# Kernel tuning notes

Hardware: AMD Instinct MI355X
Metric: run time of the kernel (lower is better)

Reference implementation:

```python
import jax, jax.numpy as jnp
import numpy as np

RADIUS = 5
KERNEL_SIZE = 2 * RADIUS - 1  # 9
PAD = KERNEL_SIZE // 2        # 4
H, W = 2048, 2048


def make_distance_kernel():
    center = RADIUS - 1
    y, x = jnp.meshgrid(jnp.arange(KERNEL_SIZE), jnp.arange(KERNEL_SIZE), indexing='ij')
    d = jnp.sqrt((x - center).astype(jnp.float32) ** 2 + (y - center).astype(jnp.float32) ** 2)
    return d.at[center, center].set(0.0)


def setup_inputs() -> dict:
    key = jax.random.key(0)
    target = (jax.random.uniform(key, (5, H, W)) < 0.15).astype(jnp.float32)
    distance_kernel = make_distance_kernel()
    return {"target": target, "distance_kernel": distance_kernel}


def _contour_weights(target, kernel):
    combined = (target.sum(axis=0) > 0).astype(jnp.float32)          # [H, W]
    padded = jnp.pad(combined, PAD, mode='edge')                      # replicate pad
    min_d = jnp.full_like(combined, jnp.inf)
    inf = jnp.float32(jnp.inf)
    for i in range(KERNEL_SIZE):
        for j in range(KERNEL_SIZE):
            if i == PAD and j == PAD:
                continue
            shifted = padded[i:i + H, j:j + W]
            diff = (shifted != combined).astype(jnp.float32)
            dist = jnp.where(diff > 0, kernel[i, j] / (diff + 1e-10), inf)
            min_d = jnp.minimum(min_d, dist)
    return jnp.where(min_d < inf, 1.0 / (min_d + 1e-10), 0.0)


def reference(target, distance_kernel):
    feature_weight = target.sum(axis=0)                               # [H, W]
    contour = _contour_weights(target, distance_kernel)
    weights = (feature_weight + contour) ** 2
    weights = (weights - weights.min()) / (weights.max() - weights.min() + 1e-10)
    return weights * (target.sum(axis=0) > 0).astype(jnp.float32)
```

## Files before the change

### kernel.cpp

```cpp
#include <hip/hip_runtime.h>
#include <stdint.h>

#define HH 2048
#define WW 2048
#define NPIX (HH*WW)
#define MROW (WW/32)
#define TSX 64
#define TSY 32
#define NBLK ((WW/TSX)*(HH/TSY))

__global__ __launch_bounds__(256) void fw_kernel(
    const float* __restrict__ target, uint8_t* __restrict__ fw,
    uint32_t* __restrict__ mask)
{
    __shared__ uint8_t nib[256];
    const int t = threadIdx.x;
    const int i = blockIdx.x * 256 + t;
    const float4* t4 = (const float4*)target;
    float4 a = t4[i];
    float4 b = t4[(NPIX/4) + i];
    float4 c = t4[2*(NPIX/4) + i];
    float4 d = t4[3*(NPIX/4) + i];
    float4 e = t4[4*(NPIX/4) + i];
    uchar4 o;
    o.x = (unsigned char)(a.x + b.x + c.x + d.x + e.x);
    o.y = (unsigned char)(a.y + b.y + c.y + d.y + e.y);
    o.z = (unsigned char)(a.z + b.z + c.z + d.z + e.z);
    o.w = (unsigned char)(a.w + b.w + c.w + d.w + e.w);
    ((uchar4*)fw)[i] = o;
    nib[t] = (uint8_t)((o.x ? 1u : 0u) | (o.y ? 2u : 0u) | (o.z ? 4u : 0u) | (o.w ? 8u : 0u));
    __syncthreads();
    if (t < 32) {
        const uint8_t* p = nib + t * 8;
        uint32_t w = 0;
        #pragma unroll
        for (int k = 0; k < 8; ++k) w |= (uint32_t)p[k] << (4 * k);
        mask[blockIdx.x * 32 + t] = w;
    }
}

__global__ __launch_bounds__(256) void contour_kernel(
    const uint8_t* __restrict__ fw, const uint32_t* __restrict__ mask,
    const float* __restrict__ dk,
    uint8_t* __restrict__ wcode, float* __restrict__ pmin, float* __restrict__ pmax)
{
    __shared__ uint32_t maskw[TSY + 8][4];
    __shared__ uint8_t  lutm2[512];
    __shared__ float    inv_ext[101];
    __shared__ float    redmn[4], redmx[4];

    const int t   = threadIdx.x;
    const int gx0 = blockIdx.x * TSX;
    const int gy0 = blockIdx.y * TSY;

    if (t < 101) inv_ext[t] = 0.0f;
    for (int idx = t; idx < 512; idx += 256) {
        uint32_t rev = __builtin_bitreverse32((uint32_t)idx) >> 23;
        uint32_t g = ((((uint32_t)idx | rev) >> 4) & 0x1Fu) | 0x100u;
        uint32_t mk = (uint32_t)__builtin_ctz(g);
        lutm2[idx] = (uint8_t)(mk * mk);
    }
    const int w0 = gx0 >> 5;
    if (t < (TSY + 8) * 4) {
        int hr = t >> 2, wc = t & 3;
        int gy = gy0 - 4 + hr; gy = min(max(gy, 0), HH - 1);
        const uint32_t* rowp = mask + gy * MROW;
        int wi = w0 - 1 + wc;
        uint32_t v;
        if (wi < 0)            v = (rowp[0] & 1u) ? 0xFFFFFFFFu : 0u;
        else if (wi > MROW-1)  v = (rowp[MROW-1] >> 31) ? 0xFFFFFFFFu : 0u;
        else                   v = rowp[wi];
        maskw[hr][wc] = v;
    }
    __syncthreads();
    if (t < 81) {
        int iy = t / 9, jx = t - (t / 9) * 9;
        int dy = iy - 4, dx = jx - 4;
        int d2 = dy * dy + dx * dx;
        if (d2 != 0)
            inv_ext[d2] = 1.0f / (dk[t] / (1.0f + 1e-10f) + 1e-10f);
    }
    __syncthreads();

    const int rl  = t >> 3;
    const int xg  = t & 7;
    const int gy  = gy0 + rl;
    const int gxb = gx0 + xg * 8;

    uint32_t fwlo = *(const uint32_t*)(fw + gy * WW + gxb);
    uint32_t fwhi = *(const uint32_t*)(fw + gy * WW + gxb + 4);

    const int pos  = xg * 8 + 28;
    const int wsel = pos >> 5;
    const uint32_t sh = (uint32_t)(pos & 31);
    uint32_t wrow[9];
    #pragma unroll
    for (int k = 0; k < 9; ++k) {
        uint64_t v = (((uint64_t)maskw[rl + k][wsel + 1]) << 32) | maskw[rl + k][wsel];
        wrow[k] = (uint32_t)(v >> sh);
    }
    uint32_t orx[4], andx[4];
    #pragma unroll
    for (int k = 1; k <= 4; ++k) {
        orx[k-1]  = wrow[4 - k] | wrow[4 + k];
        andx[k-1] = wrow[4 - k] & wrow[4 + k];
    }

    float lmn = __int_as_float(0x7F800000);
    float lmx = 0.0f;
    uint32_t outb0 = 0, outb1 = 0;

    #pragma unroll
    for (int j = 0; j < 8; ++j) {
        uint32_t craw = (wrow[4] >> (4 + j)) & 1u;
        uint32_t cm = 0u - craw;
        uint32_t x0 = ((wrow[4] ^ cm) >> j) & 0x1FFu;
        uint32_t d2m = (uint32_t)lutm2[x0];
        #pragma unroll
        for (int k = 1; k <= 4; ++k) {
            uint32_t sel = craw ? andx[k-1] : orx[k-1];
            uint32_t x = ((sel ^ cm) >> j) & 0x1FFu;
            uint32_t d2 = (uint32_t)lutm2[x] + (uint32_t)(k * k);
            d2m = min(d2m, d2);
        }
        float contour = inv_ext[d2m];
        uint32_t enc = (d2m > 32u) ? 26u : d2m;
        uint32_t fwj = (j < 4 ? (fwlo >> (8 * j)) : (fwhi >> (8 * (j - 4)))) & 0xFFu;
        uint32_t code = ((enc - 1u) << 3) | fwj;
        if (j < 4) outb0 |= code << (8 * j);
        else       outb1 |= code << (8 * (j - 4));
        float wv = (float)fwj + contour;
        wv = wv * wv;
        lmn = fminf(lmn, wv);
        lmx = fmaxf(lmx, wv);
    }
    uint2 ob; ob.x = outb0; ob.y = outb1;
    *(uint2*)(wcode + gy * WW + gxb) = ob;

    #pragma unroll
    for (int off = 32; off > 0; off >>= 1) {
        lmn = fminf(lmn, __shfl_xor(lmn, off));
        lmx = fmaxf(lmx, __shfl_xor(lmx, off));
    }
    if ((t & 63) == 0) { redmn[t >> 6] = lmn; redmx[t >> 6] = lmx; }
    __syncthreads();
    if (t == 0) {
        float mn = fminf(fminf(redmn[0], redmn[1]), fminf(redmn[2], redmn[3]));
        float mx = fmaxf(fmaxf(redmx[0], redmx[1]), fmaxf(redmx[2], redmx[3]));
        int bid = blockIdx.y * gridDim.x + blockIdx.x;
        pmin[bid] = mn;
        pmax[bid] = mx;
    }
}

__global__ __launch_bounds__(256) void norm_kernel(
    const uint8_t* __restrict__ wcode, const float* __restrict__ dk,
    const float* __restrict__ pmin, const float* __restrict__ pmax,
    float* __restrict__ out)
{
    __shared__ float ct[33];
    __shared__ float wlut[256];
    __shared__ float smn[4], smx[4];
    const int t = threadIdx.x;

    if (t < 33) ct[t] = 0.0f;
    const float4* pn4 = (const float4*)pmin;
    const float4* px4 = (const float4*)pmax;
    float4 a = pn4[t * 2], b = pn4[t * 2 + 1];
    float4 c = px4[t * 2], d = px4[t * 2 + 1];
    __syncthreads();
    if (t < 81) {
        int iy = t / 9, jx = t - (t / 9) * 9;
        int dy = iy - 4, dx = jx - 4;
        int d2 = dy * dy + dx * dx;
        if (d2 != 0) ct[d2] = 1.0f / (dk[t] / (1.0f + 1e-10f) + 1e-10f);
    }
    __syncthreads();
    {
        float wv = (float)(t & 7) + ct[(t >> 3) + 1];
        wlut[t] = wv * wv;
    }
    float mn = fminf(fminf(fminf(a.x, a.y), fminf(a.z, a.w)),
                     fminf(fminf(b.x, b.y), fminf(b.z, b.w)));
    float mx = fmaxf(fmaxf(fmaxf(c.x, c.y), fmaxf(c.z, c.w)),
                     fmaxf(fmaxf(d.x, d.y), fmaxf(d.z, d.w)));
    #pragma unroll
    for (int off = 32; off > 0; off >>= 1) {
        mn = fminf(mn, __shfl_xor(mn, off));
        mx = fmaxf(mx, __shfl_xor(mx, off));
    }
    if ((t & 63) == 0) { smn[t >> 6] = mn; smx[t >> 6] = mx; }
    __syncthreads();
    mn = fminf(fminf(smn[0], smn[1]), fminf(smn[2], smn[3]));
    mx = fmaxf(fmaxf(smx[0], smx[1]), fmaxf(smx[2], smx[3]));
    const float rden = 1.0f / (mx - mn + 1e-10f);

    const int i = blockIdx.x * 256 + t;
    uint2 cb = ((const uint2*)wcode)[i];
    uint32_t b0 = cb.x, b1 = cb.y;
    float4 o0, o1;
    o0.x = (b0 & 7u)         ? (wlut[b0 & 0xFFu] - mn) * rden         : 0.0f;
    o0.y = ((b0 >> 8) & 7u)  ? (wlut[(b0 >> 8) & 0xFFu] - mn) * rden  : 0.0f;
    o0.z = ((b0 >> 16) & 7u) ? (wlut[(b0 >> 16) & 0xFFu] - mn) * rden : 0.0f;
    o0.w = ((b0 >> 24) & 7u) ? (wlut[b0 >> 24] - mn) * rden           : 0.0f;
    o1.x = (b1 & 7u)         ? (wlut[b1 & 0xFFu] - mn) * rden         : 0.0f;
    o1.y = ((b1 >> 8) & 7u)  ? (wlut[(b1 >> 8) & 0xFFu] - mn) * rden  : 0.0f;
    o1.z = ((b1 >> 16) & 7u) ? (wlut[(b1 >> 16) & 0xFFu] - mn) * rden : 0.0f;
    o1.w = ((b1 >> 24) & 7u) ? (wlut[b1 >> 24] - mn) * rden           : 0.0f;
    ((float4*)out)[i * 2]     = o0;
    ((float4*)out)[i * 2 + 1] = o1;
}

extern "C" void kernel_launch(void* const* d_in, const int* in_sizes, int n_in,
                              void* d_out, int out_size, void* d_ws, size_t ws_size,
                              hipStream_t stream)
{
    const float* target = (const float*)d_in[0];
    const float* dk     = (const float*)d_in[1];
    float* out = (float*)d_out;

    uint8_t* wsb = (uint8_t*)d_ws;
    uint8_t*  fw    = wsb;
    uint8_t*  wcode = wsb + NPIX;
    uint32_t* mask  = (uint32_t*)(wsb + 2 * NPIX);
    float*    pmin  = (float*)(wsb + 2 * NPIX + NPIX / 8);
    float*    pmax  = pmin + NBLK;

    fw_kernel<<<NPIX / 4 / 256, 256, 0, stream>>>(target, fw, mask);

    dim3 gridB(WW / TSX, HH / TSY);
    contour_kernel<<<gridB, 256, 0, stream>>>(fw, mask, dk, wcode, pmin, pmax);

    norm_kernel<<<NPIX / 8 / 256, 256, 0, stream>>>(wcode, dk, pmin, pmax, out);
}
```

Before: 35.09 us.

## Fuse channel-sum and contour kernels into one tiled kernel with halo recompute

Merges the feature-weight/mask kernel into the contour kernel. Each 64x64 block now reads the five target channels directly, builds the bit mask in shared memory, and recomputes the halo from global memory instead of going through intermediate fw and mask buffers. Tiles grow to 64x64, and the norm kernel now reads one float4 of partials per thread instead of two. This removes a launch and the round-trip of the fw byte array and mask words, at the cost of redundant halo loads of the 5-channel input.

```diff
diff --git a/kernel.cpp b/kernel.cpp
--- a/kernel.cpp
+++ b/kernel.cpp
@@ -4,138 +4,149 @@
 #define HH 2048
 #define WW 2048
 #define NPIX (HH*WW)
-#define MROW (WW/32)
-#define TSX 64
-#define TSY 32
-#define NBLK ((WW/TSX)*(HH/TSY))
-
-__global__ __launch_bounds__(256) void fw_kernel(
-    const float* __restrict__ target, uint8_t* __restrict__ fw,
-    uint32_t* __restrict__ mask)
-{
-    __shared__ uint8_t nib[256];
-    const int t = threadIdx.x;
-    const int i = blockIdx.x * 256 + t;
-    const float4* t4 = (const float4*)target;
-    float4 a = t4[i];
-    float4 b = t4[(NPIX/4) + i];
-    float4 c = t4[2*(NPIX/4) + i];
-    float4 d = t4[3*(NPIX/4) + i];
-    float4 e = t4[4*(NPIX/4) + i];
-    uchar4 o;
-    o.x = (unsigned char)(a.x + b.x + c.x + d.x + e.x);
-    o.y = (unsigned char)(a.y + b.y + c.y + d.y + e.y);
-    o.z = (unsigned char)(a.z + b.z + c.z + d.z + e.z);
-    o.w = (unsigned char)(a.w + b.w + c.w + d.w + e.w);
-    ((uchar4*)fw)[i] = o;
-    nib[t] = (uint8_t)((o.x ? 1u : 0u) | (o.y ? 2u : 0u) | (o.z ? 4u : 0u) | (o.w ? 8u : 0u));
-    __syncthreads();
-    if (t < 32) {
-        const uint8_t* p = nib + t * 8;
-        uint32_t w = 0;
-        #pragma unroll
-        for (int k = 0; k < 8; ++k) w |= (uint32_t)p[k] << (4 * k);
-        mask[blockIdx.x * 32 + t] = w;
-    }
-}
-
-__global__ __launch_bounds__(256) void contour_kernel(
-    const uint8_t* __restrict__ fw, const uint32_t* __restrict__ mask,
-    const float* __restrict__ dk,
+#define TS 64
+#define NBX (WW/TS)
+#define NBY (HH/TS)
+#define NBLK (NBX*NBY)
+#define HR (TS+8)
+#define QW 18
+#define BST 24
+#define MW 3
+
+__global__ __launch_bounds__(256, 2) void fused_kernel(
+    const float* __restrict__ target, const float* __restrict__ dk,
     uint8_t* __restrict__ wcode, float* __restrict__ pmin, float* __restrict__ pmax)
 {
-    __shared__ uint32_t maskw[TSY + 8][4];
+    __shared__ uint8_t  bmask[HR * BST];
+    __shared__ uint32_t maskw[HR][MW];
     __shared__ uint8_t  lutm2[512];
-    __shared__ float    inv_ext[101];
+    __shared__ float    inv_ext[65];
     __shared__ float    redmn[4], redmx[4];
 
     const int t   = threadIdx.x;
-    const int gx0 = blockIdx.x * TSX;
-    const int gy0 = blockIdx.y * TSY;
-
-    if (t < 101) inv_ext[t] = 0.0f;
+    const int gx0 = blockIdx.x * TS;
+    const int gy0 = blockIdx.y * TS;
+    const float4* t4 = (const float4*)target;
+
     for (int idx = t; idx < 512; idx += 256) {
         uint32_t rev = __builtin_bitreverse32((uint32_t)idx) >> 23;
         uint32_t g = ((((uint32_t)idx | rev) >> 4) & 0x1Fu) | 0x100u;
         uint32_t mk = (uint32_t)__builtin_ctz(g);
         lutm2[idx] = (uint8_t)(mk * mk);
     }
-    const int w0 = gx0 >> 5;
-    if (t < (TSY + 8) * 4) {
-        int hr = t >> 2, wc = t & 3;
-        int gy = gy0 - 4 + hr; gy = min(max(gy, 0), HH - 1);
-        const uint32_t* rowp = mask + gy * MROW;
-        int wi = w0 - 1 + wc;
-        uint32_t v;
-        if (wi < 0)            v = (rowp[0] & 1u) ? 0xFFFFFFFFu : 0u;
-        else if (wi > MROW-1)  v = (rowp[MROW-1] >> 31) ? 0xFFFFFFFFu : 0u;
-        else                   v = rowp[wi];
-        maskw[hr][wc] = v;
-    }
-    __syncthreads();
+    if (t < 65) inv_ext[t] = 0.0f;
+    if (t < HR) {
+        uint16_t* p = (uint16_t*)(bmask + t * BST + 18);
+        p[0] = 0; p[1] = 0; p[2] = 0;
+    }
+
+    uint32_t fwl[2], fwh[2];
+    #pragma unroll
+    for (int gi = 0; gi < 2; ++gi) {
+        int g = t + gi * 256;
+        int r = g >> 3, xg = g & 7;
+        int qb = (gy0 + r) * (WW / 4) + (gx0 >> 2) + xg * 2;
+        float4 a0 = t4[qb],                 a1 = t4[qb + 1];
+        float4 b0 = t4[qb +     NPIX / 4],  b1 = t4[qb + 1 +     NPIX / 4];
+        float4 c0 = t4[qb + 2 * (NPIX/4)],  c1 = t4[qb + 1 + 2 * (NPIX/4)];
+        float4 d0 = t4[qb + 3 * (NPIX/4)],  d1 = t4[qb + 1 + 3 * (NPIX/4)];
+        float4 e0 = t4[qb + 4 * (NPIX/4)],  e1 = t4[qb + 1 + 4 * (NPIX/4)];
+        float f0 = a0.x+b0.x+c0.x+d0.x+e0.x, f1 = a0.y+b0.y+c0.y+d0.y+e0.y;
+        float f2 = a0.z+b0.z+c0.z+d0.z+e0.z, f3 = a0.w+b0.w+c0.w+d0.w+e0.w;
+        float f4 = a1.x+b1.x+c1.x+d1.x+e1.x, f5 = a1.y+b1.y+c1.y+d1.y+e1.y;
+        float f6 = a1.z+b1.z+c1.z+d1.z+e1.z, f7 = a1.w+b1.w+c1.w+d1.w+e1.w;
+        fwl[gi] = (uint32_t)f0 | ((uint32_t)f1 << 8) | ((uint32_t)f2 << 16) | ((uint32_t)f3 << 24);
+        fwh[gi] = (uint32_t)f4 | ((uint32_t)f5 << 8) | ((uint32_t)f6 << 16) | ((uint32_t)f7 << 24);
+        uint32_t nib0 = (f0!=0.f?1u:0u)|(f1!=0.f?2u:0u)|(f2!=0.f?4u:0u)|(f3!=0.f?8u:0u);
+        uint32_t nib1 = (f4!=0.f?1u:0u)|(f5!=0.f?2u:0u)|(f6!=0.f?4u:0u)|(f7!=0.f?8u:0u);
+        bmask[(4 + r) * BST + 1 + 2 * xg] = (uint8_t)nib0;
+        bmask[(4 + r) * BST + 2 + 2 * xg] = (uint8_t)nib1;
+    }
+
+    for (int idx = t; idx < 272; idx += 256) {
+        int hy, q;
+        if (idx < 144) { int h = idx / QW; q = idx - h * QW; hy = (h < 4) ? h : h + 64; }
+        else           { int j = idx - 144; hy = 4 + (j >> 1); q = (j & 1) ? (QW - 1) : 0; }
+        int gy = gy0 - 4 + hy; gy = min(max(gy, 0), HH - 1);
+        int col0 = gx0 - 4 + 4 * q;
+        int qx = col0 >> 2; qx = min(max(qx, 0), WW / 4 - 1);
+        int qb = gy * (WW / 4) + qx;
+        float4 a = t4[qb],               b = t4[qb +     NPIX / 4];
+        float4 c = t4[qb + 2*(NPIX/4)],  d = t4[qb + 3 * (NPIX/4)];
+        float4 e = t4[qb + 4*(NPIX/4)];
+        float f0 = a.x+b.x+c.x+d.x+e.x, f1 = a.y+b.y+c.y+d.y+e.y;
+        float f2 = a.z+b.z+c.z+d.z+e.z, f3 = a.w+b.w+c.w+d.w+e.w;
+        uint32_t nib = (f0!=0.f?1u:0u)|(f1!=0.f?2u:0u)|(f2!=0.f?4u:0u)|(f3!=0.f?8u:0u);
+        if (col0 < 0)    nib = (nib & 1u) * 0xFu;
+        if (col0 >= WW)  nib = (nib >> 3) * 0xFu;
+        bmask[hy * BST + q] = (uint8_t)nib;
+    }
+    __syncthreads();
+
     if (t < 81) {
         int iy = t / 9, jx = t - (t / 9) * 9;
         int dy = iy - 4, dx = jx - 4;
         int d2 = dy * dy + dx * dx;
-        if (d2 != 0)
-            inv_ext[d2] = 1.0f / (dk[t] / (1.0f + 1e-10f) + 1e-10f);
-    }
-    __syncthreads();
-
-    const int rl  = t >> 3;
-    const int xg  = t & 7;
-    const int gy  = gy0 + rl;
-    const int gxb = gx0 + xg * 8;
-
-    uint32_t fwlo = *(const uint32_t*)(fw + gy * WW + gxb);
-    uint32_t fwhi = *(const uint32_t*)(fw + gy * WW + gxb + 4);
-
-    const int pos  = xg * 8 + 28;
-    const int wsel = pos >> 5;
-    const uint32_t sh = (uint32_t)(pos & 31);
-    uint32_t wrow[9];
-    #pragma unroll
-    for (int k = 0; k < 9; ++k) {
-        uint64_t v = (((uint64_t)maskw[rl + k][wsel + 1]) << 32) | maskw[rl + k][wsel];
-        wrow[k] = (uint32_t)(v >> sh);
-    }
-    uint32_t orx[4], andx[4];
-    #pragma unroll
-    for (int k = 1; k <= 4; ++k) {
-        orx[k-1]  = wrow[4 - k] | wrow[4 + k];
-        andx[k-1] = wrow[4 - k] & wrow[4 + k];
-    }
+        if (d2 != 0) inv_ext[d2] = 1.0f / (dk[t] / (1.0f + 1e-10f) + 1e-10f);
+    }
+    if (t < HR * MW) {
+        int hy = t / MW, ws = t - (t / MW) * MW;
+        uint32_t v0 = *(const uint32_t*)(bmask + hy * BST + 8 * ws);
+        uint32_t v1 = *(const uint32_t*)(bmask + hy * BST + 8 * ws + 4);
+        v0 = (v0 | (v0 >> 4)) & 0x00FF00FFu; v0 = (v0 | (v0 >> 8)) & 0xFFFFu;
+        v1 = (v1 | (v1 >> 4)) & 0x00FF00FFu; v1 = (v1 | (v1 >> 8)) & 0xFFFFu;
+        maskw[hy][ws] = v0 | (v1 << 16);
+    }
+    __syncthreads();
 
     float lmn = __int_as_float(0x7F800000);
     float lmx = 0.0f;
-    uint32_t outb0 = 0, outb1 = 0;
-
-    #pragma unroll
-    for (int j = 0; j < 8; ++j) {
-        uint32_t craw = (wrow[4] >> (4 + j)) & 1u;
-        uint32_t cm = 0u - craw;
-        uint32_t x0 = ((wrow[4] ^ cm) >> j) & 0x1FFu;
-        uint32_t d2m = (uint32_t)lutm2[x0];
+    #pragma unroll
+    for (int gi = 0; gi < 2; ++gi) {
+        int g = t + gi * 256;
+        int r = g >> 3, xg = g & 7;
+        const int wsel = xg >> 2;
+        const uint32_t sh = (uint32_t)((8 * xg) & 31);
+        uint32_t wrow[9];
+        #pragma unroll
+        for (int k = 0; k < 9; ++k) {
+            uint64_t v = (((uint64_t)maskw[r + k][wsel + 1]) << 32) | maskw[r + k][wsel];
+            wrow[k] = (uint32_t)(v >> sh);
+        }
+        uint32_t orx[4], andx[4];
         #pragma unroll
         for (int k = 1; k <= 4; ++k) {
-            uint32_t sel = craw ? andx[k-1] : orx[k-1];
-            uint32_t x = ((sel ^ cm) >> j) & 0x1FFu;
-            uint32_t d2 = (uint32_t)lutm2[x] + (uint32_t)(k * k);
-            d2m = min(d2m, d2);
+            orx[k-1]  = wrow[4 - k] | wrow[4 + k];
+            andx[k-1] = wrow[4 - k] & wrow[4 + k];
         }
-        float contour = inv_ext[d2m];
-        uint32_t enc = (d2m > 32u) ? 26u : d2m;
-        uint32_t fwj = (j < 4 ? (fwlo >> (8 * j)) : (fwhi >> (8 * (j - 4)))) & 0xFFu;
-        uint32_t code = ((enc - 1u) << 3) | fwj;
-        if (j < 4) outb0 |= code << (8 * j);
-        else       outb1 |= code << (8 * (j - 4));
-        float wv = (float)fwj + contour;
-        wv = wv * wv;
-        lmn = fminf(lmn, wv);
-        lmx = fmaxf(lmx, wv);
-    }
-    uint2 ob; ob.x = outb0; ob.y = outb1;
-    *(uint2*)(wcode + gy * WW + gxb) = ob;
+        uint32_t outb0 = 0, outb1 = 0;
+        #pragma unroll
+        for (int j = 0; j < 8; ++j) {
+            uint32_t craw = (wrow[4] >> (4 + j)) & 1u;
+            uint32_t cm = 0u - craw;
+            uint32_t x0 = ((wrow[4] ^ cm) >> j) & 0x1FFu;
+            uint32_t d2m = (uint32_t)lutm2[x0];
+            #pragma unroll
+            for (int k = 1; k <= 4; ++k) {
+                uint32_t sel = craw ? andx[k-1] : orx[k-1];
+                uint32_t x = ((sel ^ cm) >> j) & 0x1FFu;
+                uint32_t d2 = (uint32_t)lutm2[x] + (uint32_t)(k * k);
+                d2m = min(d2m, d2);
+            }
+            float contour = inv_ext[d2m];
+            uint32_t enc = (d2m > 32u) ? 26u : d2m;
+            uint32_t fwj = (j < 4 ? (fwl[gi] >> (8 * j)) : (fwh[gi] >> (8 * (j - 4)))) & 0xFFu;
+            uint32_t code = ((enc - 1u) << 3) | fwj;
+            if (j < 4) outb0 |= code << (8 * j);
+            else       outb1 |= code << (8 * (j - 4));
+            float wv = (float)fwj + contour;
+            wv = wv * wv;
+            lmn = fminf(lmn, wv);
+            lmx = fmaxf(lmx, wv);
+        }
+        uint2 ob; ob.x = outb0; ob.y = outb1;
+        *(uint2*)(wcode + (gy0 + r) * WW + gx0 + 8 * xg) = ob;
+    }
 
     #pragma unroll
     for (int off = 32; off > 0; off >>= 1) {
@@ -147,7 +158,7 @@
     if (t == 0) {
         float mn = fminf(fminf(redmn[0], redmn[1]), fminf(redmn[2], redmn[3]));
         float mx = fmaxf(fmaxf(redmx[0], redmx[1]), fmaxf(redmx[2], redmx[3]));
-        int bid = blockIdx.y * gridDim.x + blockIdx.x;
+        int bid = blockIdx.y * NBX + blockIdx.x;
         pmin[bid] = mn;
         pmax[bid] = mx;
     }
@@ -166,8 +177,8 @@
     if (t < 33) ct[t] = 0.0f;
     const float4* pn4 = (const float4*)pmin;
     const float4* px4 = (const float4*)pmax;
-    float4 a = pn4[t * 2], b = pn4[t * 2 + 1];
-    float4 c = px4[t * 2], d = px4[t * 2 + 1];
+    float4 a = pn4[t];
+    float4 c = px4[t];
     __syncthreads();
     if (t < 81) {
         int iy = t / 9, jx = t - (t / 9) * 9;
@@ -180,10 +191,8 @@
         float wv = (float)(t & 7) + ct[(t >> 3) + 1];
         wlut[t] = wv * wv;
     }
-    float mn = fminf(fminf(fminf(a.x, a.y), fminf(a.z, a.w)),
-                     fminf(fminf(b.x, b.y), fminf(b.z, b.w)));
-    float mx = fmaxf(fmaxf(fmaxf(c.x, c.y), fmaxf(c.z, c.w)),
-                     fmaxf(fmaxf(d.x, d.y), fmaxf(d.z, d.w)));
+    float mn = fminf(fminf(a.x, a.y), fminf(a.z, a.w));
+    float mx = fmaxf(fmaxf(c.x, c.y), fmaxf(c.z, c.w));
     #pragma unroll
     for (int off = 32; off > 0; off >>= 1) {
         mn = fminf(mn, __shfl_xor(mn, off));
@@ -220,16 +229,11 @@
     float* out = (float*)d_out;
 
     uint8_t* wsb = (uint8_t*)d_ws;
-    uint8_t*  fw    = wsb;
-    uint8_t*  wcode = wsb + NPIX;
-    uint32_t* mask  = (uint32_t*)(wsb + 2 * NPIX);
-    float*    pmin  = (float*)(wsb + 2 * NPIX + NPIX / 8);
-    float*    pmax  = pmin + NBLK;
-
-    fw_kernel<<<NPIX / 4 / 256, 256, 0, stream>>>(target, fw, mask);
-
-    dim3 gridB(WW / TSX, HH / TSY);
-    contour_kernel<<<gridB, 256, 0, stream>>>(fw, mask, dk, wcode, pmin, pmax);
+    uint8_t* wcode = wsb;
+    float*   pmin  = (float*)(wsb + NPIX);
+    float*   pmax  = pmin + NBLK;
+
+    fused_kernel<<<dim3(NBX, NBY), 256, 0, stream>>>(target, dk, wcode, pmin, pmax);
 
     norm_kernel<<<NPIX / 8 / 256, 256, 0, stream>>>(wcode, dk, pmin, pmax, out);
 }
```

Result: slower. 42.05 us (+19.8%).

## Pack feature counts as nibbles and use 64x64 contour tiles with 512 threads

Applied to the files above, without the earlier changes.

The per-pixel feature sum (0-5) is now stored as a 4-bit nibble instead of a byte, which halves the intermediate fw buffer written by the first kernel and read by the contour kernel. The contour kernel's tile grows from 64x32 to 64x64 with 512 threads. Each block therefore amortises its LUT setup and halo load over more pixels, and the grid produces half as many per-block min/max partials for the norm kernel to reduce. The LUT build is done in a single pass and the fw load is issued before the first barrier so it overlaps the shared-memory setup. The cost is fewer, larger blocks, which may lower occupancy.

```diff
diff --git a/kernel.cpp b/kernel.cpp
--- a/kernel.cpp
+++ b/kernel.cpp
@@ -5,12 +5,12 @@
 #define WW 2048
 #define NPIX (HH*WW)
 #define MROW (WW/32)
-#define TSX 64
-#define TSY 32
-#define NBLK ((WW/TSX)*(HH/TSY))
+#define TS 64
+#define NBT (WW/TS)
+#define NBLK (NBT*NBT)
 
 __global__ __launch_bounds__(256) void fw_kernel(
-    const float* __restrict__ target, uint8_t* __restrict__ fw,
+    const float* __restrict__ target, uint16_t* __restrict__ fwnib,
     uint32_t* __restrict__ mask)
 {
     __shared__ uint8_t nib[256];
@@ -22,13 +22,12 @@
     float4 c = t4[2*(NPIX/4) + i];
     float4 d = t4[3*(NPIX/4) + i];
     float4 e = t4[4*(NPIX/4) + i];
-    uchar4 o;
-    o.x = (unsigned char)(a.x + b.x + c.x + d.x + e.x);
-    o.y = (unsigned char)(a.y + b.y + c.y + d.y + e.y);
-    o.z = (unsigned char)(a.z + b.z + c.z + d.z + e.z);
-    o.w = (unsigned char)(a.w + b.w + c.w + d.w + e.w);
-    ((uchar4*)fw)[i] = o;
-    nib[t] = (uint8_t)((o.x ? 1u : 0u) | (o.y ? 2u : 0u) | (o.z ? 4u : 0u) | (o.w ? 8u : 0u));
+    uint32_t f0 = (uint32_t)(a.x + b.x + c.x + d.x + e.x);
+    uint32_t f1 = (uint32_t)(a.y + b.y + c.y + d.y + e.y);
+    uint32_t f2 = (uint32_t)(a.z + b.z + c.z + d.z + e.z);
+    uint32_t f3 = (uint32_t)(a.w + b.w + c.w + d.w + e.w);
+    fwnib[i] = (uint16_t)(f0 | (f1 << 4) | (f2 << 8) | (f3 << 12));
+    nib[t] = (uint8_t)((f0 ? 1u : 0u) | (f1 ? 2u : 0u) | (f2 ? 4u : 0u) | (f3 ? 8u : 0u));
     __syncthreads();
     if (t < 32) {
         const uint8_t* p = nib + t * 8;
@@ -39,32 +38,29 @@
     }
 }
 
-__global__ __launch_bounds__(256) void contour_kernel(
-    const uint8_t* __restrict__ fw, const uint32_t* __restrict__ mask,
+__global__ __launch_bounds__(512) void contour_kernel(
+    const uint16_t* __restrict__ fwnib, const uint32_t* __restrict__ mask,
     const float* __restrict__ dk,
     uint8_t* __restrict__ wcode, float* __restrict__ pmin, float* __restrict__ pmax)
 {
-    __shared__ uint32_t maskw[TSY + 8][4];
+    __shared__ uint32_t maskw[TS + 8][4];
     __shared__ uint8_t  lutm2[512];
-    __shared__ float    inv_ext[101];
-    __shared__ float    redmn[4], redmx[4];
+    __shared__ float    inv_ext[65];
+    __shared__ float    redmn[8], redmx[8];
 
     const int t   = threadIdx.x;
-    const int gx0 = blockIdx.x * TSX;
-    const int gy0 = blockIdx.y * TSY;
-
-    if (t < 101) inv_ext[t] = 0.0f;
-    for (int idx = t; idx < 512; idx += 256) {
-        uint32_t rev = __builtin_bitreverse32((uint32_t)idx) >> 23;
-        uint32_t g = ((((uint32_t)idx | rev) >> 4) & 0x1Fu) | 0x100u;
-        uint32_t mk = (uint32_t)__builtin_ctz(g);
-        lutm2[idx] = (uint8_t)(mk * mk);
-    }
+    const int gx0 = blockIdx.x * TS;
+    const int gy0 = blockIdx.y * TS;
+    const int r   = t >> 3;
+    const int xg  = t & 7;
+    const int gy  = gy0 + r;
+    const int gxb = gx0 + 8 * xg;
+
     const int w0 = gx0 >> 5;
-    if (t < (TSY + 8) * 4) {
+    if (t < (TS + 8) * 4) {
         int hr = t >> 2, wc = t & 3;
-        int gy = gy0 - 4 + hr; gy = min(max(gy, 0), HH - 1);
-        const uint32_t* rowp = mask + gy * MROW;
+        int hgy = gy0 - 4 + hr; hgy = min(max(hgy, 0), HH - 1);
+        const uint32_t* rowp = mask + hgy * MROW;
         int wi = w0 - 1 + wc;
         uint32_t v;
         if (wi < 0)            v = (rowp[0] & 1u) ? 0xFFFFFFFFu : 0u;
@@ -72,31 +68,30 @@
         else                   v = rowp[wi];
         maskw[hr][wc] = v;
     }
+    const uint32_t fwd = *(const uint32_t*)((const uint8_t*)fwnib + gy * (WW/2) + (gxb >> 1));
+    {
+        uint32_t rev = __builtin_bitreverse32((uint32_t)t) >> 23;
+        uint32_t g = ((((uint32_t)t | rev) >> 4) & 0x1Fu) | 0x100u;
+        uint32_t mk = (uint32_t)__builtin_ctz(g);
+        lutm2[t] = (uint8_t)(mk * mk);
+    }
+    if (t < 65) inv_ext[t] = 0.0f;
     __syncthreads();
     if (t < 81) {
         int iy = t / 9, jx = t - (t / 9) * 9;
         int dy = iy - 4, dx = jx - 4;
         int d2 = dy * dy + dx * dx;
-        if (d2 != 0)
-            inv_ext[d2] = 1.0f / (dk[t] / (1.0f + 1e-10f) + 1e-10f);
-    }
-    __syncthreads();
-
-    const int rl  = t >> 3;
-    const int xg  = t & 7;
-    const int gy  = gy0 + rl;
-    const int gxb = gx0 + xg * 8;
-
-    uint32_t fwlo = *(const uint32_t*)(fw + gy * WW + gxb);
-    uint32_t fwhi = *(const uint32_t*)(fw + gy * WW + gxb + 4);
-
-    const int pos  = xg * 8 + 28;
+        if (d2 != 0) inv_ext[d2] = 1.0f / (dk[t] / (1.0f + 1e-10f) + 1e-10f);
+    }
+    __syncthreads();
+
+    const int pos  = 8 * xg + 28;
     const int wsel = pos >> 5;
     const uint32_t sh = (uint32_t)(pos & 31);
     uint32_t wrow[9];
     #pragma unroll
     for (int k = 0; k < 9; ++k) {
-        uint64_t v = (((uint64_t)maskw[rl + k][wsel + 1]) << 32) | maskw[rl + k][wsel];
+        uint64_t v = (((uint64_t)maskw[r + k][wsel + 1]) << 32) | maskw[r + k][wsel];
         wrow[k] = (uint32_t)(v >> sh);
     }
     uint32_t orx[4], andx[4];
@@ -105,11 +100,9 @@
         orx[k-1]  = wrow[4 - k] | wrow[4 + k];
         andx[k-1] = wrow[4 - k] & wrow[4 + k];
     }
-
     float lmn = __int_as_float(0x7F800000);
     float lmx = 0.0f;
     uint32_t outb0 = 0, outb1 = 0;
-
     #pragma unroll
     for (int j = 0; j < 8; ++j) {
         uint32_t craw = (wrow[4] >> (4 + j)) & 1u;
@@ -125,7 +118,7 @@
         }
         float contour = inv_ext[d2m];
         uint32_t enc = (d2m > 32u) ? 26u : d2m;
-        uint32_t fwj = (j < 4 ? (fwlo >> (8 * j)) : (fwhi >> (8 * (j - 4)))) & 0xFFu;
+        uint32_t fwj = (fwd >> (4 * j)) & 0xFu;
         uint32_t code = ((enc - 1u) << 3) | fwj;
         if (j < 4) outb0 |= code << (8 * j);
         else       outb1 |= code << (8 * (j - 4));
@@ -145,9 +138,10 @@
     if ((t & 63) == 0) { redmn[t >> 6] = lmn; redmx[t >> 6] = lmx; }
     __syncthreads();
     if (t == 0) {
-        float mn = fminf(fminf(redmn[0], redmn[1]), fminf(redmn[2], redmn[3]));
-        float mx = fmaxf(fmaxf(redmx[0], redmx[1]), fmaxf(redmx[2], redmx[3]));
-        int bid = blockIdx.y * gridDim.x + blockIdx.x;
+        float mn = redmn[0], mx = redmx[0];
+        #pragma unroll
+        for (int i = 1; i < 8; ++i) { mn = fminf(mn, redmn[i]); mx = fmaxf(mx, redmx[i]); }
+        int bid = blockIdx.y * NBT + blockIdx.x;
         pmin[bid] = mn;
         pmax[bid] = mx;
     }
@@ -166,8 +160,8 @@
     if (t < 33) ct[t] = 0.0f;
     const float4* pn4 = (const float4*)pmin;
     const float4* px4 = (const float4*)pmax;
-    float4 a = pn4[t * 2], b = pn4[t * 2 + 1];
-    float4 c = px4[t * 2], d = px4[t * 2 + 1];
+    float4 a = pn4[t];
+    float4 c = px4[t];
     __syncthreads();
     if (t < 81) {
         int iy = t / 9, jx = t - (t / 9) * 9;
@@ -180,10 +174,8 @@
         float wv = (float)(t & 7) + ct[(t >> 3) + 1];
         wlut[t] = wv * wv;
     }
-    float mn = fminf(fminf(fminf(a.x, a.y), fminf(a.z, a.w)),
-                     fminf(fminf(b.x, b.y), fminf(b.z, b.w)));
-    float mx = fmaxf(fmaxf(fmaxf(c.x, c.y), fmaxf(c.z, c.w)),
-                     fmaxf(fmaxf(d.x, d.y), fmaxf(d.z, d.w)));
+    float mn = fminf(fminf(a.x, a.y), fminf(a.z, a.w));
+    float mx = fmaxf(fmaxf(c.x, c.y), fmaxf(c.z, c.w));
     #pragma unroll
     for (int off = 32; off > 0; off >>= 1) {
         mn = fminf(mn, __shfl_xor(mn, off));
@@ -220,16 +212,15 @@
     float* out = (float*)d_out;
 
     uint8_t* wsb = (uint8_t*)d_ws;
-    uint8_t*  fw    = wsb;
-    uint8_t*  wcode = wsb + NPIX;
-    uint32_t* mask  = (uint32_t*)(wsb + 2 * NPIX);
-    float*    pmin  = (float*)(wsb + 2 * NPIX + NPIX / 8);
+    uint16_t* fwnib = (uint16_t*)wsb;
+    uint8_t*  wcode = wsb + NPIX/2;
+    uint32_t* mask  = (uint32_t*)(wsb + NPIX/2 + NPIX);
+    float*    pmin  = (float*)(wsb + NPIX/2 + NPIX + NPIX/8);
     float*    pmax  = pmin + NBLK;
 
-    fw_kernel<<<NPIX / 4 / 256, 256, 0, stream>>>(target, fw, mask);
-
-    dim3 gridB(WW / TSX, HH / TSY);
-    contour_kernel<<<gridB, 256, 0, stream>>>(fw, mask, dk, wcode, pmin, pmax);
+    fw_kernel<<<NPIX / 4 / 256, 256, 0, stream>>>(target, fwnib, mask);
+
+    contour_kernel<<<dim3(NBT, NBT), 512, 0, stream>>>(fwnib, mask, dk, wcode, pmin, pmax);
 
     norm_kernel<<<NPIX / 8 / 256, 256, 0, stream>>>(wcode, dk, pmin, pmax, out);
 }
```

Measured after the change: 36.13 us. 1.03x slower.
